# Performance work log

Measured on AMD Instinct MI355X. Metric: run time of the kernel, lower is better.

Reference implementation:

```python
import jax, jax.numpy as jnp
import numpy as np

N_NODES = 8192


def _gcn_norm(edge_index, num_nodes):
    # PyG GCNConv default: add self-loops, symmetric normalization.
    src, dst = edge_index[0], edge_index[1]
    loop = jnp.arange(num_nodes, dtype=src.dtype)
    src = jnp.concatenate([src, loop])
    dst = jnp.concatenate([dst, loop])
    deg = jax.ops.segment_sum(jnp.ones_like(dst, dtype=jnp.float32), dst,
                              num_segments=num_nodes)
    dis = jnp.where(deg > 0, jax.lax.rsqrt(jnp.maximum(deg, 1.0)), 0.0)
    norm = dis[src] * dis[dst]  # [E + N]
    return src, dst, norm


def _gcn_conv(x, W, b, src, dst, norm, num_nodes):
    h = x @ W                           # [N, F_out] dense GEMM
    msg = h[src] * norm[:, None]        # gather + scale, [E+N, F_out]
    out = jax.ops.segment_sum(msg, dst, num_segments=num_nodes)  # scatter-add
    return out + b


def setup_inputs() -> dict:
    key = jax.random.key(0)
    ks = jax.random.split(key, 8)
    N, E, F_in, H1, H2, F_out = N_NODES, 65536, 512, 4096, 1024, 10
    x = jax.random.normal(ks[0], (N, F_in), dtype=jnp.float32)
    edge_index = jax.random.randint(ks[1], (2, E), 0, N, dtype=jnp.int64)
    # Glorot-ish scaled weights
    W1 = jax.random.normal(ks[2], (F_in, H1), dtype=jnp.float32) * (1.0 / np.sqrt(F_in))
    b1 = jnp.zeros((H1,), dtype=jnp.float32)
    W2 = jax.random.normal(ks[3], (H1, H2), dtype=jnp.float32) * (1.0 / np.sqrt(H1))
    b2 = jnp.zeros((H2,), dtype=jnp.float32)
    W3 = jax.random.normal(ks[4], (H2, F_out), dtype=jnp.float32) * (1.0 / np.sqrt(H2))
    b3 = jnp.zeros((F_out,), dtype=jnp.float32)
    return {"x": x, "W1": W1, "b1": b1, "W2": W2, "b2": b2,
            "W3": W3, "b3": b3, "edge_index": edge_index}


def reference(x, W1, b1, W2, b2, W3, b3, edge_index):
    N = N_NODES
    src, dst, norm = _gcn_norm(edge_index, N)
    h = _gcn_conv(x.astype(jnp.float32), W1, b1, src, dst, norm, N)
    h = jax.nn.relu(h)  # dropout is identity in eval mode
    h = _gcn_conv(h, W2, b2, src, dst, norm, N)
    h = jax.nn.relu(h)
    h = _gcn_conv(h, W3, b3, src, dst, norm, N)
    return jax.nn.log_softmax(h, axis=1)
```

## Files before the change

kernel.cpp:

```cpp
#include <hip/hip_runtime.h>
#include <math.h>

#define N_NODES 8192
#define N_EDGES 65536
#define F_IN    512
#define HID1    4096
#define HID2    1024
#define F_OUT   10
#define H3_STRIDE 16

typedef __bf16 bf16x8 __attribute__((ext_vector_type(8)));
typedef float floatx16 __attribute__((ext_vector_type(16)));

static __device__ __forceinline__ unsigned short f2bf(float f) {
    union { float f; unsigned u; } v; v.f = f;
    unsigned r = v.u + 0x7fffu + ((v.u >> 16) & 1u);
    return (unsigned short)(r >> 16);
}
static __device__ __forceinline__ void unpack8(uint4 r, float* f) {
    union { unsigned u; float v; } c;
    c.u = r.x << 16;          f[0] = c.v;
    c.u = r.x & 0xffff0000u;  f[1] = c.v;
    c.u = r.y << 16;          f[2] = c.v;
    c.u = r.y & 0xffff0000u;  f[3] = c.v;
    c.u = r.z << 16;          f[4] = c.v;
    c.u = r.z & 0xffff0000u;  f[5] = c.v;
    c.u = r.w << 16;          f[6] = c.v;
    c.u = r.w & 0xffff0000u;  f[7] = c.v;
}
static __device__ __forceinline__ uint4 pack8(const float* f) {
    uint4 o;
    o.x = (unsigned)f2bf(f[0]) | ((unsigned)f2bf(f[1]) << 16);
    o.y = (unsigned)f2bf(f[2]) | ((unsigned)f2bf(f[3]) << 16);
    o.z = (unsigned)f2bf(f[4]) | ((unsigned)f2bf(f[5]) << 16);
    o.w = (unsigned)f2bf(f[6]) | ((unsigned)f2bf(f[7]) << 16);
    return o;
}

__global__ __launch_bounds__(1024) void hist_scan_kernel(
        const int* __restrict__ ei, int* __restrict__ deg,
        int* __restrict__ row_ptr, int* __restrict__ cnt) {
    __shared__ int hist[N_NODES];
    __shared__ int sums[1024];
    int t = threadIdx.x;
#pragma unroll
    for (int i = 0; i < 8; i++) hist[t + i * 1024] = 0;
    __syncthreads();
    const int4* ei4 = (const int4*)(ei + N_EDGES);
#pragma unroll
    for (int i = 0; i < 16; i++) {
        int4 d4 = ei4[i * 1024 + t];
        atomicAdd(&hist[d4.x], 1);
        atomicAdd(&hist[d4.y], 1);
        atomicAdd(&hist[d4.z], 1);
        atomicAdd(&hist[d4.w], 1);
    }
    __syncthreads();
    int base = t * 8;
    int local[8], run = 0;
#pragma unroll
    for (int i = 0; i < 8; i++) {
        int dv = hist[base + i];
        deg[base + i] = dv;
        cnt[base + i] = 0;
        local[i] = run; run += dv;
    }
    sums[t] = run;
    __syncthreads();
    for (int off = 1; off < 1024; off <<= 1) {
        int val = (t >= off) ? sums[t - off] : 0;
        __syncthreads();
        sums[t] += val;
        __syncthreads();
    }
    int offset = (t == 0) ? 0 : sums[t - 1];
#pragma unroll
    for (int i = 0; i < 8; i++) row_ptr[base + i] = offset + local[i];
    if (t == 1023) row_ptr[N_NODES] = sums[1023];
}

static __device__ __forceinline__ void transpose_body(
        const float* __restrict__ W, unsigned short* __restrict__ Wt,
        int K, int N, int k0, int n0, int tid, float (*t)[33]) {
    int c = tid & 31, r8 = tid >> 5;
#pragma unroll
    for (int i = 0; i < 4; i++) {
        int r = r8 + i * 8;
        t[r][c] = W[(size_t)(k0 + r) * N + n0 + c];
    }
    __syncthreads();
#pragma unroll
    for (int i = 0; i < 4; i++) {
        int r = r8 + i * 8;
        Wt[(size_t)(n0 + r) * K + k0 + c] = f2bf(t[c][r]);
    }
}

__global__ __launch_bounds__(256) void megaprep_kernel(
        const int* __restrict__ ei, const int* __restrict__ deg,
        const int* __restrict__ row_ptr, int* __restrict__ cnt,
        int* __restrict__ csr_src, float* __restrict__ csr_w,
        const float* __restrict__ x, unsigned short* __restrict__ xb,
        const float* __restrict__ W1, unsigned short* __restrict__ W1t,
        const float* __restrict__ W2, unsigned short* __restrict__ W2t) {
    __shared__ float t[32][33];
    int b = blockIdx.x, tid = threadIdx.x;
    if (b < 256) {
        int e = b * 256 + tid;
        int s = ei[e];
        int d = ei[N_EDGES + e];
        int slot = row_ptr[d] + atomicAdd(&cnt[d], 1);
        csr_src[slot] = s;
        csr_w[slot] = rsqrtf((float)((deg[s] + 1) * (deg[d] + 1)));
    } else if (b < 4352) {
        int i = (b - 256) * 256 + tid;
        float4 a = ((const float4*)x)[i];
        ushort4 o;
        o.x = f2bf(a.x); o.y = f2bf(a.y); o.z = f2bf(a.z); o.w = f2bf(a.w);
        ((ushort4*)xb)[i] = o;
    } else if (b < 6400) {
        int bb = b - 4352;
        transpose_body(W1, W1t, F_IN, HID1, (bb >> 7) * 32, (bb & 127) * 32, tid, t);
    } else {
        int bb = b - 6400;
        transpose_body(W2, W2t, HID1, HID2, (bb >> 5) * 32, (bb & 31) * 32, tid, t);
    }
}

__global__ __launch_bounds__(256) void agg1_sliced_kernel(
        const unsigned short* __restrict__ xb, const int* __restrict__ row_ptr,
        const int* __restrict__ csr_src, const float* __restrict__ csr_w,
        const int* __restrict__ deg, unsigned short* __restrict__ out) {
    int b = blockIdx.x;
    int slice = b & 3;
    int ng = b >> 2;
    int v = ng * 4 + (threadIdx.x >> 6);
    int lane = threadIdx.x & 63;
    int sbase = slice * 64 + lane;
    const unsigned* xu = (const unsigned*)xb;
    float sw = 1.0f / (float)(deg[v] + 1);
    union { unsigned u; float f; } cv;
    unsigned su = xu[(size_t)v * 256 + sbase];
    float a0, a1;
    cv.u = su << 16;          a0 = sw * cv.f;
    cv.u = su & 0xffff0000u;  a1 = sw * cv.f;
    int e = row_ptr[v], end = row_ptr[v + 1];
    for (; e + 4 <= end; e += 4) {
        int s0 = csr_src[e],     s1 = csr_src[e + 1];
        int s2 = csr_src[e + 2], s3 = csr_src[e + 3];
        float w0 = csr_w[e],     w1 = csr_w[e + 1];
        float w2 = csr_w[e + 2], w3 = csr_w[e + 3];
        unsigned u0 = xu[(size_t)s0 * 256 + sbase];
        unsigned u1 = xu[(size_t)s1 * 256 + sbase];
        unsigned u2 = xu[(size_t)s2 * 256 + sbase];
        unsigned u3 = xu[(size_t)s3 * 256 + sbase];
        cv.u = u0 << 16; a0 += w0 * cv.f;  cv.u = u0 & 0xffff0000u; a1 += w0 * cv.f;
        cv.u = u1 << 16; a0 += w1 * cv.f;  cv.u = u1 & 0xffff0000u; a1 += w1 * cv.f;
        cv.u = u2 << 16; a0 += w2 * cv.f;  cv.u = u2 & 0xffff0000u; a1 += w2 * cv.f;
        cv.u = u3 << 16; a0 += w3 * cv.f;  cv.u = u3 & 0xffff0000u; a1 += w3 * cv.f;
    }
    for (; e < end; e++) {
        int s = csr_src[e]; float w = csr_w[e];
        unsigned u0 = xu[(size_t)s * 256 + sbase];
        cv.u = u0 << 16; a0 += w * cv.f;  cv.u = u0 & 0xffff0000u; a1 += w * cv.f;
    }
    ((unsigned*)out)[(size_t)v * 256 + sbase] =
        (unsigned)f2bf(a0) | ((unsigned)f2bf(a1) << 16);
}

__global__ __launch_bounds__(256) void agg2_gemm3_sliced_kernel(
        const unsigned short* __restrict__ h, const int* __restrict__ row_ptr,
        const int* __restrict__ csr_src, const float* __restrict__ csr_w,
        const int* __restrict__ deg, const float* __restrict__ b2,
        const float* __restrict__ W3, float* __restrict__ h3p) {
    int b = blockIdx.x;
    int slice = b & 7;
    int ng = b >> 3;
    int v = ng * 4 + (threadIdx.x >> 6);
    int lane = threadIdx.x & 63;
    int sbase = slice * 64 + lane;
    int f0 = slice * 128 + lane * 2;
    const unsigned* hu = (const unsigned*)h;
    float w3r0[F_OUT], w3r1[F_OUT];
#pragma unroll
    for (int c = 0; c < F_OUT; c++) {
        w3r0[c] = W3[(size_t)f0 * F_OUT + c];
        w3r1[c] = W3[(size_t)(f0 + 1) * F_OUT + c];
    }
    float bv0 = b2[f0], bv1 = b2[f0 + 1];
    float sw = 1.0f / (float)(deg[v] + 1);
    union { unsigned u; float f; } cv;
    unsigned su = hu[(size_t)v * 512 + sbase];
    float a0, a1;
    cv.u = su << 16;          a0 = sw * cv.f;
    cv.u = su & 0xffff0000u;  a1 = sw * cv.f;
    int e = row_ptr[v], end = row_ptr[v + 1];
    for (; e + 4 <= end; e += 4) {
        int s0 = csr_src[e],     s1 = csr_src[e + 1];
        int s2 = csr_src[e + 2], s3 = csr_src[e + 3];
        float w0 = csr_w[e],     w1 = csr_w[e + 1];
        float w2 = csr_w[e + 2], w3 = csr_w[e + 3];
        unsigned u0 = hu[(size_t)s0 * 512 + sbase];
        unsigned u1 = hu[(size_t)s1 * 512 + sbase];
        unsigned u2 = hu[(size_t)s2 * 512 + sbase];
        unsigned u3 = hu[(size_t)s3 * 512 + sbase];
        cv.u = u0 << 16; a0 += w0 * cv.f;  cv.u = u0 & 0xffff0000u; a1 += w0 * cv.f;
        cv.u = u1 << 16; a0 += w1 * cv.f;  cv.u = u1 & 0xffff0000u; a1 += w1 * cv.f;
        cv.u = u2 << 16; a0 += w2 * cv.f;  cv.u = u2 & 0xffff0000u; a1 += w2 * cv.f;
        cv.u = u3 << 16; a0 += w3 * cv.f;  cv.u = u3 & 0xffff0000u; a1 += w3 * cv.f;
    }
    for (; e < end; e++) {
        int s = csr_src[e]; float w = csr_w[e];
        unsigned u0 = hu[(size_t)s * 512 + sbase];
        cv.u = u0 << 16; a0 += w * cv.f;  cv.u = u0 & 0xffff0000u; a1 += w * cv.f;
    }
    a0 = fmaxf(a0 + bv0, 0.0f);
    a1 = fmaxf(a1 + bv1, 0.0f);
    float partial[F_OUT];
#pragma unroll
    for (int c = 0; c < F_OUT; c++) partial[c] = a0 * w3r0[c] + a1 * w3r1[c];
#pragma unroll
    for (int c = 0; c < F_OUT; c++) {
#pragma unroll
        for (int off = 32; off > 0; off >>= 1)
            partial[c] += __shfl_xor(partial[c], off, 64);
    }
    if (lane == 0) {
        float* dst = h3p + ((size_t)slice * N_NODES + v) * H3_STRIDE;
#pragma unroll
        for (int c = 0; c < F_OUT; c++) dst[c] = partial[c];
    }
}

__global__ __launch_bounds__(256) void reduce_h3_kernel(
        const float* __restrict__ h3p, float* __restrict__ h3) {
    int idx = blockIdx.x * 256 + threadIdx.x;
    int v = idx >> 2, g = idx & 3;
    const float4* p4 = (const float4*)h3p;
    float4 s = make_float4(0.f, 0.f, 0.f, 0.f);
#pragma unroll
    for (int sl = 0; sl < 8; sl++) {
        float4 a = p4[((size_t)sl * N_NODES + v) * 4 + g];
        s.x += a.x; s.y += a.y; s.z += a.z; s.w += a.w;
    }
    ((float4*)h3)[(size_t)v * 4 + g] = s;
}

#define P8_OFF(R_, lc_) ((((R_) >> 2) * 128) + (((((R_) & 3) << 2) | (lc_)) ^ (((R_) >> 2) & 3)) * 8)

#define Q4_STAGE(Lbuf_, base_, k0_) do {                                       \
    unsigned short* L_ = (Lbuf_);                                              \
    _Pragma("unroll")                                                          \
    for (int j = 0; j < 2; j++) {                                              \
        int sl = j * 512 + tid;                                                \
        int s4 = sl >> 4, cs = sl & 15;                                        \
        int csp = cs ^ (s4 & 3);                                               \
        int grow = s4 * 4 + (csp >> 2);                                        \
        int gcol = (csp & 3) * 8;                                              \
        __builtin_amdgcn_global_load_lds(                                      \
            (const __attribute__((address_space(1))) void*)((base_) + (size_t)grow * K + (k0_) + gcol), \
            (__attribute__((address_space(3))) void*)(&L_[sl * 8]), 16, 0, 0); \
    }                                                                          \
} while (0)

#define P8_STAGE(mat_, kh_, dd_, base_, k0_) \
    Q4_STAGE(lds + ((dd_) * 4 + (mat_) * 2 + (kh_)) * 8192, base_, (k0_) + (kh_) * 32)

#define P8_MAIN_LOOP(NT_)                                                      \
    P8_STAGE(0, 0, 0, Abase, 0);                                               \
    P8_STAGE(1, 0, 0, Bbase, 0);                                               \
    P8_STAGE(0, 1, 0, Abase, 0);                                               \
    P8_STAGE(1, 1, 0, Bbase, 0);                                               \
    asm volatile("s_waitcnt vmcnt(4)" ::: "memory");                           \
    __builtin_amdgcn_s_barrier();                                              \
    for (int t = 0; t < (NT_); t++) {                                          \
        int d = t & 1, dn = d ^ 1;                                             \
        int k1 = (t + 1) * 64;                                                 \
        _Pragma("unroll")                                                      \
        for (int kk = 0; kk < 4; kk++) {                                       \
            if (kk == 2) {                                                     \
                if (t + 1 < (NT_))                                             \
                    asm volatile("s_waitcnt vmcnt(4)" ::: "memory");           \
                else                                                           \
                    asm volatile("s_waitcnt vmcnt(0)" ::: "memory");           \
                __builtin_amdgcn_s_barrier();                                  \
            }                                                                  \
            int kh = kk >> 1;                                                  \
            int lc0 = (kk & 1) * 2 + lhalf;                                    \
            const unsigned short* Ak = lds + (d * 4 + kh) * 8192;              \
            const unsigned short* Bk = lds + (d * 4 + 2 + kh) * 8192;          \
            bf16x8 af[4], bfr[2];                                              \
            _Pragma("unroll")                                                  \
            for (int mt = 0; mt < 4; mt++) {                                   \
                int R = wm * 128 + mt * 32 + lrow;                             \
                af[mt] = *(const bf16x8*)&Ak[P8_OFF(R, lc0)];                  \
            }                                                                  \
            _Pragma("unroll")                                                  \
            for (int nt = 0; nt < 2; nt++) {                                   \
                int R = wn * 64 + nt * 32 + lrow;                              \
                bfr[nt] = *(const bf16x8*)&Bk[P8_OFF(R, lc0)];                 \
            }                                                                  \
            if (t + 1 < (NT_)) {                                               \
                if (kk == 0)      P8_STAGE(0, 0, dn, Abase, k1);               \
                else if (kk == 1) P8_STAGE(1, 0, dn, Bbase, k1);               \
                else if (kk == 2) P8_STAGE(0, 1, dn, Abase, k1);               \
                else              P8_STAGE(1, 1, dn, Bbase, k1);               \
            }                                                                  \
            __builtin_amdgcn_s_barrier();                                      \
            __builtin_amdgcn_s_setprio(1);                                     \
            _Pragma("unroll")                                                  \
            for (int mt = 0; mt < 4; mt++)                                     \
                _Pragma("unroll")                                              \
                for (int nt = 0; nt < 2; nt++)                                 \
                    acc[mt][nt] = __builtin_amdgcn_mfma_f32_32x32x16_bf16(     \
                        af[mt], bfr[nt], acc[mt][nt], 0, 0, 0);                \
            __builtin_amdgcn_s_setprio(0);                                     \
            if (kk == 0 || kk == 2) __builtin_amdgcn_s_barrier();              \
        }                                                                      \
        asm volatile("s_waitcnt vmcnt(4)" ::: "memory");                       \
        __builtin_amdgcn_s_barrier();                                          \
    }

__global__ __launch_bounds__(512, 2) void gemm1_pipe8_kernel(
        const unsigned short* __restrict__ A,
        const unsigned short* __restrict__ Bt,
        const float* __restrict__ bias,
        unsigned short* __restrict__ C) {
    __shared__ unsigned short lds[65536];
    const int K = F_IN, N = HID1;
    int tid = threadIdx.x;
    int wave = tid >> 6, lane = tid & 63;
    int wm = wave >> 2, wn = wave & 3;
    int lrow = lane & 31, lhalf = lane >> 5;

    int b = blockIdx.x;
    int GN = HID1 >> 8;
    int ntile = (b >> 3) % GN;
    int mtile = ((b >> 3) / GN) * 8 + (b & 7);
    int m0 = mtile * 256, n0 = ntile * 256;

    const unsigned short* Abase = A + (size_t)m0 * K;
    const unsigned short* Bbase = Bt + (size_t)n0 * K;

    floatx16 acc[4][2] = {};
    P8_MAIN_LOOP(8)

#pragma unroll
    for (int mt = 0; mt < 4; mt++) {
#pragma unroll
        for (int nt = 0; nt < 2; nt++) {
            int col = n0 + wn * 64 + nt * 32 + lrow;
            float bv = bias[col];
#pragma unroll
            for (int reg = 0; reg < 16; reg++) {
                int row = m0 + wm * 128 + mt * 32 + (reg & 3) + 8 * (reg >> 2) + 4 * lhalf;
                float v = fmaxf(acc[mt][nt][reg] + bv, 0.0f);
                C[(size_t)row * N + col] = f2bf(v);
            }
        }
    }
}

__global__ __launch_bounds__(512, 2) void gemm2_q4_split_kernel(
        const unsigned short* __restrict__ A,
        const unsigned short* __restrict__ Bt,
        unsigned short* __restrict__ Ca,
        unsigned short* __restrict__ Cb) {
    __shared__ unsigned short lds[65536];
    const int K = HID1;
    const int N = HID2;
    int tid = threadIdx.x;
    int wave = tid >> 6, lane = tid & 63;
    int wm = wave >> 2, wn = wave & 3;
    int lrow = lane & 31, lhalf = lane >> 5;

    int b = blockIdx.x;
    int u = b >> 3;
    int col = u & 7;
    int mtile = (u >> 3) * 8 + (b & 7);
    int ntile = col >> 1;
    int ksp = col & 1;
    int m0 = mtile * 256, n0 = ntile * 256;
    int koff = ksp * (HID1 / 2);

    const unsigned short* Abase = A + (size_t)m0 * K + koff;
    const unsigned short* Bbase = Bt + (size_t)n0 * K + koff;
    unsigned short* Cout = ksp ? Cb : Ca;

    floatx16 acc[4][2] = {};
    const int NT = (HID1 / 2) >> 5;

    Q4_STAGE(lds + 0 * 16384, Abase, 0);  Q4_STAGE(lds + 0 * 16384 + 8192, Bbase, 0);
    Q4_STAGE(lds + 1 * 16384, Abase, 32); Q4_STAGE(lds + 1 * 16384 + 8192, Bbase, 32);
    Q4_STAGE(lds + 2 * 16384, Abase, 64); Q4_STAGE(lds + 2 * 16384 + 8192, Bbase, 64);
    asm volatile("s_waitcnt vmcnt(8)" ::: "memory");
    __builtin_amdgcn_s_barrier();

    for (int t = 0; t < NT; t++) {
        const unsigned short* Ak = lds + (size_t)(t & 3) * 16384;
        const unsigned short* Bk = Ak + 8192;
        unsigned short* Lnext = lds + (size_t)((t + 3) & 3) * 16384;
        int k3 = (t + 3) * 32;
#pragma unroll
        for (int kk = 0; kk < 2; kk++) {
            int lc0 = kk * 2 + lhalf;
            bf16x8 af[4], bfr[2];
#pragma unroll
            for (int mt = 0; mt < 4; mt++) {
                int R = wm * 128 + mt * 32 + lrow;
                af[mt] = *(const bf16x8*)&Ak[P8_OFF(R, lc0)];
            }
#pragma unroll
            for (int nt = 0; nt < 2; nt++) {
                int R = wn * 64 + nt * 32 + lrow;
                bfr[nt] = *(const bf16x8*)&Bk[P8_OFF(R, lc0)];
            }
            if (t + 3 < NT) {
                if (kk == 0) Q4_STAGE(Lnext, Abase, k3);
                else         Q4_STAGE(Lnext + 8192, Bbase, k3);
            }
            __builtin_amdgcn_s_setprio(1);
#pragma unroll
            for (int mt = 0; mt < 4; mt++)
#pragma unroll
                for (int nt = 0; nt < 2; nt++)
                    acc[mt][nt] = __builtin_amdgcn_mfma_f32_32x32x16_bf16(
                        af[mt], bfr[nt], acc[mt][nt], 0, 0, 0);
            __builtin_amdgcn_s_setprio(0);
        }
        if (t + 3 < NT)
            asm volatile("s_waitcnt vmcnt(8)" ::: "memory");
        else if (t + 2 < NT)
            asm volatile("s_waitcnt vmcnt(4)" ::: "memory");
        else if (t + 1 < NT)
            asm volatile("s_waitcnt vmcnt(0)" ::: "memory");
        __builtin_amdgcn_s_barrier();
    }

#pragma unroll
    for (int mt = 0; mt < 4; mt++) {
#pragma unroll
        for (int nt = 0; nt < 2; nt++) {
            int colc = n0 + wn * 64 + nt * 32 + lrow;
#pragma unroll
            for (int reg = 0; reg < 16; reg++) {
                int row = m0 + wm * 128 + mt * 32 + (reg & 3) + 8 * (reg >> 2) + 4 * lhalf;
                Cout[(size_t)row * N + colc] = f2bf(acc[mt][nt][reg]);
            }
        }
    }
}

__global__ __launch_bounds__(256) void merge_kernel(
        const unsigned short* __restrict__ Ca, unsigned short* __restrict__ Cb) {
    const uint4* a4 = (const uint4*)Ca;
    uint4* b4 = (uint4*)Cb;
    int base = blockIdx.x * 1024 + threadIdx.x;
#pragma unroll
    for (int j = 0; j < 4; j++) {
        int i = base + j * 256;
        float fa[8], fb[8];
        unpack8(a4[i], fa);
        unpack8(b4[i], fb);
#pragma unroll
        for (int k = 0; k < 8; k++) fa[k] += fb[k];
        b4[i] = pack8(fa);
    }
}

__global__ void final_kernel(const float* __restrict__ h3, const int* __restrict__ row_ptr,
                             const int* __restrict__ csr_src, const float* __restrict__ csr_w,
                             const int* __restrict__ deg, const float* __restrict__ b3,
                             float* __restrict__ out) {
    int v = blockIdx.x * blockDim.x + threadIdx.x;
    if (v >= N_NODES) return;
    const float4* h4 = (const float4*)h3;
    float sw = 1.0f / (float)(deg[v] + 1);
    float a[12];
    *(float4*)&a[0] = h4[v * 4];
    *(float4*)&a[4] = h4[v * 4 + 1];
    *(float4*)&a[8] = h4[v * 4 + 2];
    float acc[F_OUT];
#pragma unroll
    for (int c = 0; c < F_OUT; c++) acc[c] = b3[c] + sw * a[c];
    int end = row_ptr[v + 1];
    for (int e = row_ptr[v]; e < end; e++) {
        int s = csr_src[e];
        float w = csr_w[e];
        float bsrc[12];
        *(float4*)&bsrc[0] = h4[s * 4];
        *(float4*)&bsrc[4] = h4[s * 4 + 1];
        *(float4*)&bsrc[8] = h4[s * 4 + 2];
#pragma unroll
        for (int c = 0; c < F_OUT; c++) acc[c] += w * bsrc[c];
    }
    float m = acc[0];
#pragma unroll
    for (int c = 1; c < F_OUT; c++) m = fmaxf(m, acc[c]);
    float ssum = 0.0f;
#pragma unroll
    for (int c = 0; c < F_OUT; c++) ssum += expf(acc[c] - m);
    float l = logf(ssum);
#pragma unroll
    for (int c = 0; c < F_OUT; c++) out[v * F_OUT + c] = acc[c] - m - l;
}

extern "C" void kernel_launch(void* const* d_in, const int* in_sizes, int n_in,
                              void* d_out, int out_size, void* d_ws, size_t ws_size,
                              hipStream_t stream) {
    const float* x  = (const float*)d_in[0];
    const float* W1 = (const float*)d_in[1];
    const float* b1 = (const float*)d_in[2];
    const float* W2 = (const float*)d_in[3];
    const float* b2 = (const float*)d_in[4];
    const float* W3 = (const float*)d_in[5];
    const float* b3 = (const float*)d_in[6];
    const int*   ei = (const int*)d_in[7];
    float* out = (float*)d_out;

    char* p = (char*)d_ws;
    int*   deg     = (int*)p;    p += N_NODES * 4;
    int*   cnt     = (int*)p;    p += N_NODES * 4;
    int*   row_ptr = (int*)p;    p += 33024;
    int*   csr_src = (int*)p;    p += N_EDGES * 4;
    float* csr_w   = (float*)p;  p += N_EDGES * 4;
    float* h3      = (float*)p;  p += N_NODES * H3_STRIDE * 4;
    unsigned short* xb    = (unsigned short*)p; p += (size_t)N_NODES * F_IN * 2;
    unsigned short* agg_x = (unsigned short*)p; p += (size_t)N_NODES * F_IN * 2;
    unsigned short* W1t   = (unsigned short*)p; p += (size_t)HID1 * F_IN * 2;
    unsigned short* W2t   = (unsigned short*)p; p += (size_t)HID2 * HID1 * 2;
    unsigned short* h1    = (unsigned short*)p; p += (size_t)N_NODES * HID1 * 2;
    unsigned short* h2pre = (unsigned short*)p; p += (size_t)N_NODES * HID2 * 2;
    unsigned short* h2a = xb;
    float* h3p = (float*)xb;

    hist_scan_kernel<<<1, 1024, 0, stream>>>(ei, deg, row_ptr, cnt);
    megaprep_kernel<<<10496, 256, 0, stream>>>(ei, deg, row_ptr, cnt, csr_src, csr_w,
                                               x, xb, W1, W1t, W2, W2t);

    agg1_sliced_kernel<<<N_NODES / 4 * 4, 256, 0, stream>>>(
        xb, row_ptr, csr_src, csr_w, deg, agg_x);
    gemm1_pipe8_kernel<<<(N_NODES / 256) * (HID1 / 256), 512, 0, stream>>>(
        agg_x, W1t, b1, h1);

    gemm2_q4_split_kernel<<<256, 512, 0, stream>>>(h1, W2t, h2a, h2pre);
    merge_kernel<<<1024, 256, 0, stream>>>(h2a, h2pre);

    agg2_gemm3_sliced_kernel<<<N_NODES / 4 * 8, 256, 0, stream>>>(
        h2pre, row_ptr, csr_src, csr_w, deg, b2, W3, h3p);
    reduce_h3_kernel<<<N_NODES * 4 / 256, 256, 0, stream>>>(h3p, h3);

    final_kernel<<<N_NODES / 256, 256, 0, stream>>>(h3, row_ptr, csr_src, csr_w, deg, b3, out);
}
```

Measured before the change: 291.2 us.

## Retile GEMM2 to 128x256 blocks with 4 waves and triple-buffered LDS

Replaces the 256x256-tile, 8-wave GEMM2 split-K kernel with a 128x256-tile, 4-wave variant. Each wave now covers all 128 rows and a 64-column slice. The LDS pipeline drops from a 4-stage to a 3-stage ring with smaller buffers, which frees shared memory so more blocks can be resident, and the grid doubles to 512 blocks to fill more CUs. In exchange, A-operand reuse per block is lower, so global traffic for the B operand rises, and the prefetch distance is shorter.

```diff
diff --git a/kernel.cpp b/kernel.cpp
--- a/kernel.cpp
+++ b/kernel.cpp
@@ -361,17 +361,47 @@
     }
 }
 
-__global__ __launch_bounds__(512, 2) void gemm2_q4_split_kernel(
+#define DC_STAGE_A(Lbuf_, base_, k0_) do {                                     \
+    unsigned short* L_ = (Lbuf_);                                              \
+    _Pragma("unroll")                                                          \
+    for (int j = 0; j < 2; j++) {               \
+        int sl = j * 256 + tid;                                                \
+        int s4 = sl >> 4, cs = sl & 15;                                        \
+        int csp = cs ^ (s4 & 3);                                               \
+        int grow = s4 * 4 + (csp >> 2);                                        \
+        int gcol = (csp & 3) * 8;                                              \
+        __builtin_amdgcn_global_load_lds(                                      \
+            (const __attribute__((address_space(1))) void*)((base_) + (size_t)grow * K + (k0_) + gcol), \
+            (__attribute__((address_space(3))) void*)(&L_[sl * 8]), 16, 0, 0); \
+    }                                                                          \
+} while (0)
+
+#define DC_STAGE_B(Lbuf_, base_, k0_) do {                                     \
+    unsigned short* L_ = (Lbuf_);                                              \
+    _Pragma("unroll")                                                          \
+    for (int j = 0; j < 4; j++) {              \
+        int sl = j * 256 + tid;                                                \
+        int s4 = sl >> 4, cs = sl & 15;                                        \
+        int csp = cs ^ (s4 & 3);                                               \
+        int grow = s4 * 4 + (csp >> 2);                                        \
+        int gcol = (csp & 3) * 8;                                              \
+        __builtin_amdgcn_global_load_lds(                                      \
+            (const __attribute__((address_space(1))) void*)((base_) + (size_t)grow * K + (k0_) + gcol), \
+            (__attribute__((address_space(3))) void*)(&L_[sl * 8]), 16, 0, 0); \
+    }                                                                          \
+} while (0)
+
+__global__ __launch_bounds__(256, 2) void gemm2_dc_split_kernel(
         const unsigned short* __restrict__ A,
         const unsigned short* __restrict__ Bt,
         unsigned short* __restrict__ Ca,
         unsigned short* __restrict__ Cb) {
-    __shared__ unsigned short lds[65536];
+    __shared__ unsigned short lds[36864];
     const int K = HID1;
     const int N = HID2;
     int tid = threadIdx.x;
     int wave = tid >> 6, lane = tid & 63;
-    int wm = wave >> 2, wn = wave & 3;
+    int wn = wave;
     int lrow = lane & 31, lhalf = lane >> 5;
 
     int b = blockIdx.x;
@@ -380,7 +410,7 @@
     int mtile = (u >> 3) * 8 + (b & 7);
     int ntile = col >> 1;
     int ksp = col & 1;
-    int m0 = mtile * 256, n0 = ntile * 256;
+    int m0 = mtile * 128, n0 = ntile * 256;
     int koff = ksp * (HID1 / 2);
 
     const unsigned short* Abase = A + (size_t)m0 * K + koff;
@@ -390,24 +420,24 @@
     floatx16 acc[4][2] = {};
     const int NT = (HID1 / 2) >> 5;
 
-    Q4_STAGE(lds + 0 * 16384, Abase, 0);  Q4_STAGE(lds + 0 * 16384 + 8192, Bbase, 0);
-    Q4_STAGE(lds + 1 * 16384, Abase, 32); Q4_STAGE(lds + 1 * 16384 + 8192, Bbase, 32);
-    Q4_STAGE(lds + 2 * 16384, Abase, 64); Q4_STAGE(lds + 2 * 16384 + 8192, Bbase, 64);
-    asm volatile("s_waitcnt vmcnt(8)" ::: "memory");
+    DC_STAGE_A(lds + 0 * 12288, Abase, 0);  DC_STAGE_B(lds + 0 * 12288 + 4096, Bbase, 0);
+    DC_STAGE_A(lds + 1 * 12288, Abase, 32); DC_STAGE_B(lds + 1 * 12288 + 4096, Bbase, 32);
+    asm volatile("s_waitcnt vmcnt(6)" ::: "memory");
     __builtin_amdgcn_s_barrier();
 
+    int q = 0, qn = 2;
     for (int t = 0; t < NT; t++) {
-        const unsigned short* Ak = lds + (size_t)(t & 3) * 16384;
-        const unsigned short* Bk = Ak + 8192;
-        unsigned short* Lnext = lds + (size_t)((t + 3) & 3) * 16384;
-        int k3 = (t + 3) * 32;
+        const unsigned short* Ak = lds + q * 12288;
+        const unsigned short* Bk = Ak + 4096;
+        unsigned short* Lnext = lds + qn * 12288;
+        int k2 = (t + 2) * 32;
 #pragma unroll
         for (int kk = 0; kk < 2; kk++) {
             int lc0 = kk * 2 + lhalf;
             bf16x8 af[4], bfr[2];
 #pragma unroll
             for (int mt = 0; mt < 4; mt++) {
-                int R = wm * 128 + mt * 32 + lrow;
+                int R = mt * 32 + lrow;
                 af[mt] = *(const bf16x8*)&Ak[P8_OFF(R, lc0)];
             }
 #pragma unroll
@@ -415,9 +445,9 @@
                 int R = wn * 64 + nt * 32 + lrow;
                 bfr[nt] = *(const bf16x8*)&Bk[P8_OFF(R, lc0)];
             }
-            if (t + 3 < NT) {
-                if (kk == 0) Q4_STAGE(Lnext, Abase, k3);
-                else         Q4_STAGE(Lnext + 8192, Bbase, k3);
+            if (t + 2 < NT) {
+                if (kk == 0) DC_STAGE_A(Lnext, Abase, k2);
+                else         DC_STAGE_B(Lnext + 4096, Bbase, k2);
             }
             __builtin_amdgcn_s_setprio(1);
 #pragma unroll
@@ -428,13 +458,13 @@
                         af[mt], bfr[nt], acc[mt][nt], 0, 0, 0);
             __builtin_amdgcn_s_setprio(0);
         }
-        if (t + 3 < NT)
-            asm volatile("s_waitcnt vmcnt(8)" ::: "memory");
-        else if (t + 2 < NT)
-            asm volatile("s_waitcnt vmcnt(4)" ::: "memory");
+        if (t + 2 < NT)
+            asm volatile("s_waitcnt vmcnt(6)" ::: "memory");
         else if (t + 1 < NT)
             asm volatile("s_waitcnt vmcnt(0)" ::: "memory");
         __builtin_amdgcn_s_barrier();
+        q = (q == 2) ? 0 : q + 1;
+        qn = (qn == 2) ? 0 : qn + 1;
     }
 
 #pragma unroll
@@ -444,7 +474,7 @@
             int colc = n0 + wn * 64 + nt * 32 + lrow;
 #pragma unroll
             for (int reg = 0; reg < 16; reg++) {
-                int row = m0 + wm * 128 + mt * 32 + (reg & 3) + 8 * (reg >> 2) + 4 * lhalf;
+                int row = m0 + mt * 32 + (reg & 3) + 8 * (reg >> 2) + 4 * lhalf;
                 Cout[(size_t)row * N + colc] = f2bf(acc[mt][nt][reg]);
             }
         }
@@ -543,7 +573,7 @@
     gemm1_pipe8_kernel<<<(N_NODES / 256) * (HID1 / 256), 512, 0, stream>>>(
         agg_x, W1t, b1, h1);
 
-    gemm2_q4_split_kernel<<<256, 512, 0, stream>>>(h1, W2t, h2a, h2pre);
+    gemm2_dc_split_kernel<<<512, 256, 0, stream>>>(h1, W2t, h2a, h2pre);
     merge_kernel<<<1024, 256, 0, stream>>>(h2a, h2pre);
 
     agg2_gemm3_sliced_kernel<<<N_NODES / 4 * 8, 256, 0, stream>>>(
```

After: 299.2 us. +2.8%, slower.

## Overlap degree histogram with conversion work and split CSR fill into own kernel

Applied to the files above, without the earlier changes.

Moves the single-block histogram and scan into block 0 of the prep kernel, so it runs concurrently with the x conversion and weight transposes rather than serializing ahead of them. The CSR fill, which depends on row_ptr, becomes a small separate kernel launched afterward. The kernel count stays the same. The tradeoff is that the histogram now runs in a single 256-thread block doing 4x more work per thread, which may become the critical path of the prep kernel.

```diff
diff --git a/kernel.cpp b/kernel.cpp
--- a/kernel.cpp
+++ b/kernel.cpp
@@ -37,48 +37,6 @@
     return o;
 }
 
-__global__ __launch_bounds__(1024) void hist_scan_kernel(
-        const int* __restrict__ ei, int* __restrict__ deg,
-        int* __restrict__ row_ptr, int* __restrict__ cnt) {
-    __shared__ int hist[N_NODES];
-    __shared__ int sums[1024];
-    int t = threadIdx.x;
-#pragma unroll
-    for (int i = 0; i < 8; i++) hist[t + i * 1024] = 0;
-    __syncthreads();
-    const int4* ei4 = (const int4*)(ei + N_EDGES);
-#pragma unroll
-    for (int i = 0; i < 16; i++) {
-        int4 d4 = ei4[i * 1024 + t];
-        atomicAdd(&hist[d4.x], 1);
-        atomicAdd(&hist[d4.y], 1);
-        atomicAdd(&hist[d4.z], 1);
-        atomicAdd(&hist[d4.w], 1);
-    }
-    __syncthreads();
-    int base = t * 8;
-    int local[8], run = 0;
-#pragma unroll
-    for (int i = 0; i < 8; i++) {
-        int dv = hist[base + i];
-        deg[base + i] = dv;
-        cnt[base + i] = 0;
-        local[i] = run; run += dv;
-    }
-    sums[t] = run;
-    __syncthreads();
-    for (int off = 1; off < 1024; off <<= 1) {
-        int val = (t >= off) ? sums[t - off] : 0;
-        __syncthreads();
-        sums[t] += val;
-        __syncthreads();
-    }
-    int offset = (t == 0) ? 0 : sums[t - 1];
-#pragma unroll
-    for (int i = 0; i < 8; i++) row_ptr[base + i] = offset + local[i];
-    if (t == 1023) row_ptr[N_NODES] = sums[1023];
-}
-
 static __device__ __forceinline__ void transpose_body(
         const float* __restrict__ W, unsigned short* __restrict__ Wt,
         int K, int N, int k0, int n0, int tid, float (*t)[33]) {
@@ -96,35 +54,78 @@
     }
 }
 
-__global__ __launch_bounds__(256) void megaprep_kernel(
-        const int* __restrict__ ei, const int* __restrict__ deg,
-        const int* __restrict__ row_ptr, int* __restrict__ cnt,
-        int* __restrict__ csr_src, float* __restrict__ csr_w,
+__global__ __launch_bounds__(256) void prep_kernel(
+        const int* __restrict__ ei, int* __restrict__ deg,
+        int* __restrict__ row_ptr, int* __restrict__ cnt,
         const float* __restrict__ x, unsigned short* __restrict__ xb,
         const float* __restrict__ W1, unsigned short* __restrict__ W1t,
         const float* __restrict__ W2, unsigned short* __restrict__ W2t) {
-    __shared__ float t[32][33];
+    __shared__ int smem[8448];
     int b = blockIdx.x, tid = threadIdx.x;
-    if (b < 256) {
-        int e = b * 256 + tid;
-        int s = ei[e];
-        int d = ei[N_EDGES + e];
-        int slot = row_ptr[d] + atomicAdd(&cnt[d], 1);
-        csr_src[slot] = s;
-        csr_w[slot] = rsqrtf((float)((deg[s] + 1) * (deg[d] + 1)));
-    } else if (b < 4352) {
-        int i = (b - 256) * 256 + tid;
+    if (b == 0) {
+        int* hist = smem;
+        int* sums = smem + 8192;
+        int t = tid;
+#pragma unroll
+        for (int i = 0; i < 32; i++) hist[t + i * 256] = 0;
+        __syncthreads();
+        const int4* ei4 = (const int4*)(ei + N_EDGES);
+#pragma unroll
+        for (int i = 0; i < 64; i++) {
+            int4 d4 = ei4[i * 256 + t];
+            atomicAdd(&hist[d4.x], 1);
+            atomicAdd(&hist[d4.y], 1);
+            atomicAdd(&hist[d4.z], 1);
+            atomicAdd(&hist[d4.w], 1);
+        }
+        __syncthreads();
+        int base = t * 32;
+        int run = 0;
+        for (int i = 0; i < 32; i++) run += hist[base + i];
+        sums[t] = run;
+        __syncthreads();
+        for (int off = 1; off < 256; off <<= 1) {
+            int val = (t >= off) ? sums[t - off] : 0;
+            __syncthreads();
+            sums[t] += val;
+            __syncthreads();
+        }
+        run = (t == 0) ? 0 : sums[t - 1];
+        for (int i = 0; i < 32; i++) {
+            int dv = hist[base + i];
+            deg[base + i] = dv;
+            cnt[base + i] = 0;
+            row_ptr[base + i] = run;
+            run += dv;
+        }
+        if (t == 255) row_ptr[N_NODES] = run;
+    } else if (b <= 4096) {
+        int i = (b - 1) * 256 + tid;
         float4 a = ((const float4*)x)[i];
         ushort4 o;
         o.x = f2bf(a.x); o.y = f2bf(a.y); o.z = f2bf(a.z); o.w = f2bf(a.w);
         ((ushort4*)xb)[i] = o;
-    } else if (b < 6400) {
-        int bb = b - 4352;
-        transpose_body(W1, W1t, F_IN, HID1, (bb >> 7) * 32, (bb & 127) * 32, tid, t);
+    } else if (b <= 6144) {
+        int bb = b - 4097;
+        transpose_body(W1, W1t, F_IN, HID1, (bb >> 7) * 32, (bb & 127) * 32,
+                       tid, (float(*)[33])smem);
     } else {
-        int bb = b - 6400;
-        transpose_body(W2, W2t, HID1, HID2, (bb >> 5) * 32, (bb & 31) * 32, tid, t);
-    }
+        int bb = b - 6145;
+        transpose_body(W2, W2t, HID1, HID2, (bb >> 5) * 32, (bb & 31) * 32,
+                       tid, (float(*)[33])smem);
+    }
+}
+
+__global__ __launch_bounds__(256) void csr_fill_kernel(
+        const int* __restrict__ ei, const int* __restrict__ deg,
+        const int* __restrict__ row_ptr, int* __restrict__ cnt,
+        int* __restrict__ csr_src, float* __restrict__ csr_w) {
+    int e = blockIdx.x * 256 + threadIdx.x;
+    int s = ei[e];
+    int d = ei[N_EDGES + e];
+    int slot = row_ptr[d] + atomicAdd(&cnt[d], 1);
+    csr_src[slot] = s;
+    csr_w[slot] = rsqrtf((float)((deg[s] + 1) * (deg[d] + 1)));
 }
 
 __global__ __launch_bounds__(256) void agg1_sliced_kernel(
@@ -534,9 +535,9 @@
     unsigned short* h2a = xb;
     float* h3p = (float*)xb;
 
-    hist_scan_kernel<<<1, 1024, 0, stream>>>(ei, deg, row_ptr, cnt);
-    megaprep_kernel<<<10496, 256, 0, stream>>>(ei, deg, row_ptr, cnt, csr_src, csr_w,
-                                               x, xb, W1, W1t, W2, W2t);
+    prep_kernel<<<10241, 256, 0, stream>>>(ei, deg, row_ptr, cnt,
+                                           x, xb, W1, W1t, W2, W2t);
+    csr_fill_kernel<<<256, 256, 0, stream>>>(ei, deg, row_ptr, cnt, csr_src, csr_w);
 
     agg1_sliced_kernel<<<N_NODES / 4 * 4, 256, 0, stream>>>(
         xb, row_ptr, csr_src, csr_w, deg, agg_x);
```

Measured after the change: 307.7 us. 5.6% more time.

## Overlap histogram scan with conversion and transposes in one prep launch

Applied to the files above, without the earlier changes.

The single-block histogram/scan is moved into block 0 of a combined 1024-thread prep kernel, so it runs alongside the x bf16 conversion and the W1/W2 transposes instead of serialising before them. The CSR fill becomes its own small kernel launched afterwards, since it depends on the scan output. Transpose blocks now handle four 32x32 tiles each in partitioned shared memory. The goal is to hide the latency of the serial scan block, at the cost of larger blocks with more shared memory, which may lower occupancy for the conversion and transpose work.

```diff
diff --git a/kernel.cpp b/kernel.cpp
--- a/kernel.cpp
+++ b/kernel.cpp
@@ -37,48 +37,6 @@
     return o;
 }
 
-__global__ __launch_bounds__(1024) void hist_scan_kernel(
-        const int* __restrict__ ei, int* __restrict__ deg,
-        int* __restrict__ row_ptr, int* __restrict__ cnt) {
-    __shared__ int hist[N_NODES];
-    __shared__ int sums[1024];
-    int t = threadIdx.x;
-#pragma unroll
-    for (int i = 0; i < 8; i++) hist[t + i * 1024] = 0;
-    __syncthreads();
-    const int4* ei4 = (const int4*)(ei + N_EDGES);
-#pragma unroll
-    for (int i = 0; i < 16; i++) {
-        int4 d4 = ei4[i * 1024 + t];
-        atomicAdd(&hist[d4.x], 1);
-        atomicAdd(&hist[d4.y], 1);
-        atomicAdd(&hist[d4.z], 1);
-        atomicAdd(&hist[d4.w], 1);
-    }
-    __syncthreads();
-    int base = t * 8;
-    int local[8], run = 0;
-#pragma unroll
-    for (int i = 0; i < 8; i++) {
-        int dv = hist[base + i];
-        deg[base + i] = dv;
-        cnt[base + i] = 0;
-        local[i] = run; run += dv;
-    }
-    sums[t] = run;
-    __syncthreads();
-    for (int off = 1; off < 1024; off <<= 1) {
-        int val = (t >= off) ? sums[t - off] : 0;
-        __syncthreads();
-        sums[t] += val;
-        __syncthreads();
-    }
-    int offset = (t == 0) ? 0 : sums[t - 1];
-#pragma unroll
-    for (int i = 0; i < 8; i++) row_ptr[base + i] = offset + local[i];
-    if (t == 1023) row_ptr[N_NODES] = sums[1023];
-}
-
 static __device__ __forceinline__ void transpose_body(
         const float* __restrict__ W, unsigned short* __restrict__ Wt,
         int K, int N, int k0, int n0, int tid, float (*t)[33]) {
@@ -96,35 +54,81 @@
     }
 }
 
-__global__ __launch_bounds__(256) void megaprep_kernel(
-        const int* __restrict__ ei, const int* __restrict__ deg,
-        const int* __restrict__ row_ptr, int* __restrict__ cnt,
-        int* __restrict__ csr_src, float* __restrict__ csr_w,
+__global__ __launch_bounds__(1024) void prep_kernel(
+        const int* __restrict__ ei, int* __restrict__ deg,
+        int* __restrict__ row_ptr, int* __restrict__ cnt,
         const float* __restrict__ x, unsigned short* __restrict__ xb,
         const float* __restrict__ W1, unsigned short* __restrict__ W1t,
         const float* __restrict__ W2, unsigned short* __restrict__ W2t) {
-    __shared__ float t[32][33];
+    __shared__ int smem[9216];
     int b = blockIdx.x, tid = threadIdx.x;
-    if (b < 256) {
-        int e = b * 256 + tid;
-        int s = ei[e];
-        int d = ei[N_EDGES + e];
-        int slot = row_ptr[d] + atomicAdd(&cnt[d], 1);
-        csr_src[slot] = s;
-        csr_w[slot] = rsqrtf((float)((deg[s] + 1) * (deg[d] + 1)));
-    } else if (b < 4352) {
-        int i = (b - 256) * 256 + tid;
+    if (b == 0) {
+        int* hist = smem;
+        int* sums = smem + 8192;
+        int t = tid;
+#pragma unroll
+        for (int i = 0; i < 8; i++) hist[t + i * 1024] = 0;
+        __syncthreads();
+        const int4* ei4 = (const int4*)(ei + N_EDGES);
+#pragma unroll
+        for (int i = 0; i < 16; i++) {
+            int4 d4 = ei4[i * 1024 + t];
+            atomicAdd(&hist[d4.x], 1);
+            atomicAdd(&hist[d4.y], 1);
+            atomicAdd(&hist[d4.z], 1);
+            atomicAdd(&hist[d4.w], 1);
+        }
+        __syncthreads();
+        int base = t * 8;
+        int local[8], run = 0;
+#pragma unroll
+        for (int i = 0; i < 8; i++) {
+            int dv = hist[base + i];
+            deg[base + i] = dv;
+            cnt[base + i] = 0;
+            local[i] = run; run += dv;
+        }
+        sums[t] = run;
+        __syncthreads();
+        for (int off = 1; off < 1024; off <<= 1) {
+            int val = (t >= off) ? sums[t - off] : 0;
+            __syncthreads();
+            sums[t] += val;
+            __syncthreads();
+        }
+        int offset = (t == 0) ? 0 : sums[t - 1];
+#pragma unroll
+        for (int i = 0; i < 8; i++) row_ptr[base + i] = offset + local[i];
+        if (t == 1023) row_ptr[N_NODES] = sums[1023];
+    } else if (b <= 1024) {
+        int i = (b - 1) * 1024 + tid;
         float4 a = ((const float4*)x)[i];
         ushort4 o;
         o.x = f2bf(a.x); o.y = f2bf(a.y); o.z = f2bf(a.z); o.w = f2bf(a.w);
         ((ushort4*)xb)[i] = o;
-    } else if (b < 6400) {
-        int bb = b - 4352;
-        transpose_body(W1, W1t, F_IN, HID1, (bb >> 7) * 32, (bb & 127) * 32, tid, t);
+    } else if (b <= 1536) {
+        int tt = (b - 1025) * 4 + (tid >> 8);
+        float (*tg)[33] = (float(*)[33])(smem + (tid >> 8) * 1056);
+        transpose_body(W1, W1t, F_IN, HID1, (tt >> 7) * 32, (tt & 127) * 32,
+                       tid & 255, tg);
     } else {
-        int bb = b - 6400;
-        transpose_body(W2, W2t, HID1, HID2, (bb >> 5) * 32, (bb & 31) * 32, tid, t);
-    }
+        int tt = (b - 1537) * 4 + (tid >> 8);
+        float (*tg)[33] = (float(*)[33])(smem + (tid >> 8) * 1056);
+        transpose_body(W2, W2t, HID1, HID2, (tt >> 5) * 32, (tt & 31) * 32,
+                       tid & 255, tg);
+    }
+}
+
+__global__ __launch_bounds__(256) void csr_fill_kernel(
+        const int* __restrict__ ei, const int* __restrict__ deg,
+        const int* __restrict__ row_ptr, int* __restrict__ cnt,
+        int* __restrict__ csr_src, float* __restrict__ csr_w) {
+    int e = blockIdx.x * 256 + threadIdx.x;
+    int s = ei[e];
+    int d = ei[N_EDGES + e];
+    int slot = row_ptr[d] + atomicAdd(&cnt[d], 1);
+    csr_src[slot] = s;
+    csr_w[slot] = rsqrtf((float)((deg[s] + 1) * (deg[d] + 1)));
 }
 
 __global__ __launch_bounds__(256) void agg1_sliced_kernel(
@@ -534,9 +538,9 @@
     unsigned short* h2a = xb;
     float* h3p = (float*)xb;
 
-    hist_scan_kernel<<<1, 1024, 0, stream>>>(ei, deg, row_ptr, cnt);
-    megaprep_kernel<<<10496, 256, 0, stream>>>(ei, deg, row_ptr, cnt, csr_src, csr_w,
-                                               x, xb, W1, W1t, W2, W2t);
+    prep_kernel<<<2561, 1024, 0, stream>>>(ei, deg, row_ptr, cnt,
+                                           x, xb, W1, W1t, W2, W2t);
+    csr_fill_kernel<<<256, 256, 0, stream>>>(ei, deg, row_ptr, cnt, csr_src, csr_w);
 
     agg1_sliced_kernel<<<N_NODES / 4 * 4, 256, 0, stream>>>(
         xb, row_ptr, csr_src, csr_w, deg, agg_x);
```

After: 294.9 us. About the same (+1.2%).
